# Optimization experiments

Hardware: AMD Instinct MI355X
Metric: run time of the kernel (lower is better)

The kernel has to match this reference:

```python
import jax, jax.numpy as jnp
import numpy as np

BETA = 1e10  # hard softmax temperature from the original module


def setup_inputs() -> dict:
    key = jax.random.key(0)
    ks = jax.random.split(key, 7)
    bs, nc, units, feat = 128, 1024, 512, 512
    return {
        "x": jax.random.normal(ks[0], (bs, feat), jnp.float32),
        "class_logits": jax.random.normal(ks[1], (bs, nc), jnp.float32),
        "h_states": jax.random.normal(ks[2], (nc, units), jnp.float32) * 0.1,
        "c_states": jax.random.normal(ks[3], (nc, units), jnp.float32) * 0.1,
        "kernel": jax.random.normal(ks[4], (feat, 4 * units), jnp.float32) * 0.05,
        "rec_kernel": jax.random.normal(ks[5], (units, 4 * units), jnp.float32) * 0.05,
        "bias": jnp.zeros((4 * units,), jnp.float32),
    }


def _diff_scatter(A, B, w):
    # A: (nc, u) old class states, B: (bs, u) new states, w: (bs, nc) hard softmax.
    # Faithful to tf version: broadcast to (nc, bs, u), blend, then reduce_max over bs.
    m = w.T[:, :, None]                       # (nc, bs, 1)
    blended = A[:, None, :] * (1.0 - m) + B[None, :, :] * m  # (nc, bs, u)
    return jnp.max(blended, axis=1)           # (nc, u)


def reference(x, class_logits, h_states, c_states, kernel, rec_kernel, bias):
    # diff_gather: softmax-weighted sum over classes == weights @ params
    w = jax.nn.softmax(class_logits * BETA, axis=-1)  # (bs, nc), ~one-hot
    h0 = w @ h_states                                  # (bs, u)
    c0 = w @ c_states                                  # (bs, u)

    # single-step Keras LSTM (seq_len == 1): gate order i, f, c, o
    z = x @ kernel + h0 @ rec_kernel + bias            # (bs, 4u)
    i, f, g, o = jnp.split(z, 4, axis=-1)
    i = jax.nn.sigmoid(i)
    f = jax.nn.sigmoid(f)
    g = jnp.tanh(g)
    o = jax.nn.sigmoid(o)
    c = f * c0 + i * g
    h = o * jnp.tanh(c)                                # LSTM output == h

    new_h = _diff_scatter(h_states, h, w)
    new_c = _diff_scatter(c_states, c, w)
    return h, new_h, new_c
```

## Files before the change

kernel.cpp:

```cpp
#include <hip/hip_runtime.h>
#include <hip/hip_bf16.h>
#include <math.h>

#define BS    128
#define NC    1024
#define UNITS 512
#define FEAT  512
#define FOURU 2048
#define KG    4
#define NT    32
#define WPAD  40

typedef short  bf16x8 __attribute__((ext_vector_type(8)));
typedef float  f32x4  __attribute__((ext_vector_type(4)));

__device__ __forceinline__ unsigned short bf_rhu(float f) {
    union { float f; unsigned u; } v; v.f = f;
    return (unsigned short)((v.u + 0x8000u) >> 16);
}
__device__ __forceinline__ unsigned pack2(float a, float b) {
    return (unsigned)bf_rhu(a) | ((unsigned)bf_rhu(b) << 16);
}

__global__ __launch_bounds__(256) void argmax_prep_kernel(
    const float* __restrict__ logits, const float* __restrict__ x,
    const float* __restrict__ h_states,
    int* __restrict__ sidx, unsigned* __restrict__ Abf )
{
    int b = blockIdx.x;
    int t = threadIdx.x;
    float best = -INFINITY; int bi = 0;
    for (int i = t; i < NC; i += 256) {
        float v = logits[b * NC + i];
        if (v > best) { best = v; bi = i; }
    }
    for (int off = 32; off > 0; off >>= 1) {
        float ov = __shfl_down(best, off);
        int   oi = __shfl_down(bi, off);
        if (ov > best || (ov == best && oi < bi)) { best = ov; bi = oi; }
    }
    __shared__ float sv[4]; __shared__ int si[4];
    __shared__ int sbi;
    int wid = t >> 6;
    if ((t & 63) == 0) { sv[wid] = best; si[wid] = bi; }
    __syncthreads();
    if (t == 0) {
        for (int w = 1; w < 4; ++w)
            if (sv[w] > best || (sv[w] == best && si[w] < bi)) { best = sv[w]; bi = si[w]; }
        sidx[b] = bi;
        sbi = bi;
    }
    __syncthreads();
    int st = t & 127;
    const float* srcrow = (t < 128) ? (x + (long)b * FEAT)
                                    : (h_states + (long)sbi * UNITS);
    float4 v = *(const float4*)(srcrow + st * 4);
    unsigned lo = pack2(v.x, v.y), hi = pack2(v.z, v.w);
    unsigned du = (unsigned)b * 512u + (t < 128 ? 0u : 256u) + (unsigned)st * 2u;
    *(uint2*)(Abf + du) = make_uint2(lo, hi);
}

__global__ __launch_bounds__(256) void gemm_kernel(
    const unsigned short* __restrict__ Abf,
    const float* __restrict__ kern, const float* __restrict__ reck,
    float* __restrict__ z_part)
{
    __shared__ __align__(16) unsigned short as[BS * 32];
    __shared__ __align__(16) unsigned short wst[NT * WPAD];

    int t = threadIdx.x;
    int ntile = blockIdx.x * NT;
    int kg = blockIdx.y;
    const float* W = (kg < 2) ? kern : reck;
    int wk0base = (kg & 1) * 256;
    int k0base  = kg * 256;

    int wid = t >> 6, lane = t & 63;
    int l15 = lane & 15, quad = lane >> 4;

    f32x4 zero = {0.f, 0.f, 0.f, 0.f};
    f32x4 acc[2][2] = {{zero, zero}, {zero, zero}};

    #pragma unroll
    for (int kstep = 0; kstep < 8; ++kstep) {
        int k0  = k0base  + kstep * 32;
        int wk0 = wk0base + kstep * 32;

        for (int r = 0; r < 2; ++r) {
            int G = r * 256 + t;
            int m = G >> 2;
            int p = G & 3;
            int c = (p ^ (m >> 1)) & 3;
            bf16x8 v = *(const bf16x8*)(Abf + (long)m * 1024 + k0 + c * 8);
            *(bf16x8*)&as[G * 8] = v;
        }
        for (int p = 0; p < 4; ++p) {
            int kk = (t >> 5) + p * 8;
            int n  = t & 31;
            wst[n * WPAD + kk] = bf_rhu(W[(long)(wk0 + kk) * FOURU + ntile + n]);
        }
        __syncthreads();

        bf16x8 afrag[2], bfrag[2];
        for (int ms = 0; ms < 2; ++ms) {
            int m = wid * 32 + ms * 16 + l15;
            afrag[ms] = *(const bf16x8*)&as[(m * 4 + ((quad ^ (m >> 1)) & 3)) * 8];
        }
        for (int ns = 0; ns < 2; ++ns) {
            int n = ns * 16 + l15;
            bfrag[ns] = *(const bf16x8*)&wst[n * WPAD + quad * 8];
        }
        for (int ms = 0; ms < 2; ++ms)
            for (int ns = 0; ns < 2; ++ns)
                acc[ms][ns] = __builtin_amdgcn_mfma_f32_16x16x32_bf16(
                                  afrag[ms], bfrag[ns], acc[ms][ns], 0, 0, 0);
        __syncthreads();
    }

    float* zp = z_part + (long)kg * BS * FOURU;
    #pragma unroll
    for (int ms = 0; ms < 2; ++ms)
        #pragma unroll
        for (int ns = 0; ns < 2; ++ns)
            #pragma unroll
            for (int r = 0; r < 4; ++r) {
                int m = wid * 32 + ms * 16 + quad * 4 + r;
                int n = ntile + ns * 16 + l15;
                zp[(long)m * FOURU + n] = acc[ms][ns][r];
            }
}

__global__ __launch_bounds__(256) void scatter_lstm_kernel(
    const float* __restrict__ z_part, const float* __restrict__ bias,
    const float* __restrict__ h_states, const float* __restrict__ c_states,
    const int* __restrict__ sidx,
    float* __restrict__ h_out, float* __restrict__ out_h, float* __restrict__ out_c)
{
    __shared__ int s[BS];
    int t = threadIdx.x;
    if (t < BS) s[t] = sidx[t];
    __syncthreads();
    int j = blockIdx.x >> 1;
    int u = (blockIdx.x & 1) * 256 + t;

    float ah = h_states[(long)j * UNITS + u];
    float ac = c_states[(long)j * UNITS + u];

    float mh = -INFINITY, mc = -INFINITY;
    int count = 0;
    float bi_ = bias[u], bf_ = bias[512 + u], bg_ = bias[1024 + u], bo_ = bias[1536 + u];

    for (int b = 0; b < BS; ++b) {
        if (s[b] == j) {
            ++count;
            float zi = bi_, zf = bf_, zg = bg_, zo = bo_;
            #pragma unroll
            for (int kg = 0; kg < KG; ++kg) {
                const float* zp = z_part + (long)kg * BS * FOURU + (long)b * FOURU;
                zi += zp[u];
                zf += zp[512 + u];
                zg += zp[1024 + u];
                zo += zp[1536 + u];
            }
            float ig = 1.f / (1.f + expf(-zi));
            float fg = 1.f / (1.f + expf(-zf));
            float gg = tanhf(zg);
            float og = 1.f / (1.f + expf(-zo));
            float c  = fg * ac + ig * gg;
            float h  = og * tanhf(c);
            h_out[(long)b * UNITS + u] = h;
            mh = fmaxf(mh, h);
            mc = fmaxf(mc, c);
        }
    }
    out_h[(long)j * UNITS + u] = (count == BS) ? mh : fmaxf(ah, mh);
    out_c[(long)j * UNITS + u] = (count == BS) ? mc : fmaxf(ac, mc);
}

extern "C" void kernel_launch(void* const* d_in, const int* in_sizes, int n_in,
                              void* d_out, int out_size, void* d_ws, size_t ws_size,
                              hipStream_t stream)
{
    (void)in_sizes; (void)n_in; (void)out_size; (void)ws_size;
    const float* x      = (const float*)d_in[0];
    const float* logits = (const float*)d_in[1];
    const float* h_st   = (const float*)d_in[2];
    const float* c_st   = (const float*)d_in[3];
    const float* kern   = (const float*)d_in[4];
    const float* reck   = (const float*)d_in[5];
    const float* bias   = (const float*)d_in[6];

    float* out        = (float*)d_out;
    float* out_h_step = out;
    float* out_newh   = out + BS * UNITS;
    float* out_newc   = out + BS * UNITS + NC * UNITS;

    char*     ws     = (char*)d_ws;
    int*      sidx   = (int*)ws;
    unsigned* Abf    = (unsigned*)(ws + 1024);
    float*    z_part = (float*)(ws + 1024 * 1024);

    argmax_prep_kernel<<<BS, 256, 0, stream>>>(logits, x, h_st, sidx, Abf);
    gemm_kernel<<<dim3(FOURU / NT, KG), 256, 0, stream>>>(
        (const unsigned short*)Abf, kern, reck, z_part);
    scatter_lstm_kernel<<<NC * UNITS / 256, 256, 0, stream>>>(
        z_part, bias, h_st, c_st, sidx, out_h_step, out_newh, out_newc);
}
```

Baseline: 111.1 us.

## Pre-transpose weights to bf16 in prep kernel and drop LDS staging in GEMM

The prep kernel gains extra blocks that convert both weight matrices to bf16 in a transposed (n-major, k-contiguous) layout in the workspace. The GEMM then loads A and W fragments straight from global memory with no shared-memory staging or barriers. The K split grows from 4 to 8 groups, so the scatter kernel sums 8 partial results, giving more GEMM blocks. In exchange the weights are written to and read back from the workspace each call, adding an extra pass over them, and the scatter has more partials to read.

```diff
diff --git a/kernel.cpp b/kernel.cpp
--- a/kernel.cpp
+++ b/kernel.cpp
@@ -7,12 +7,10 @@
 #define UNITS 512
 #define FEAT  512
 #define FOURU 2048
-#define KG    4
-#define NT    32
-#define WPAD  40
-
-typedef short  bf16x8 __attribute__((ext_vector_type(8)));
-typedef float  f32x4  __attribute__((ext_vector_type(4)));
+#define KG    8
+
+typedef short bf16x8 __attribute__((ext_vector_type(8)));
+typedef float f32x4  __attribute__((ext_vector_type(4)));
 
 __device__ __forceinline__ unsigned short bf_rhu(float f) {
     union { float f; unsigned u; } v; v.f = f;
@@ -22,99 +20,96 @@
     return (unsigned)bf_rhu(a) | ((unsigned)bf_rhu(b) << 16);
 }
 
-__global__ __launch_bounds__(256) void argmax_prep_kernel(
+__global__ __launch_bounds__(256) void prep_kernel(
     const float* __restrict__ logits, const float* __restrict__ x,
-    const float* __restrict__ h_states,
-    int* __restrict__ sidx, unsigned* __restrict__ Abf )
-{
-    int b = blockIdx.x;
-    int t = threadIdx.x;
-    float best = -INFINITY; int bi = 0;
-    for (int i = t; i < NC; i += 256) {
-        float v = logits[b * NC + i];
-        if (v > best) { best = v; bi = i; }
+    const float* __restrict__ h_st,
+    const float* __restrict__ kern, const float* __restrict__ reck,
+    int* __restrict__ sidx,
+    unsigned short* __restrict__ Abf,
+    unsigned short* __restrict__ Wt)
+{
+    const int bid = blockIdx.x, t = threadIdx.x;
+    const int wid = t >> 6, lane = t & 63;
+
+    if (bid < BS) {
+        int b = bid;
+        float best = -INFINITY; int bi = 0;
+        for (int i = t; i < NC; i += 256) {
+            float v = logits[b * NC + i];
+            if (v > best) { best = v; bi = i; }
+        }
+        for (int off = 32; off > 0; off >>= 1) {
+            float ov = __shfl_down(best, off);
+            int   oi = __shfl_down(bi, off);
+            if (ov > best || (ov == best && oi < bi)) { best = ov; bi = oi; }
+        }
+        __shared__ float sv[4]; __shared__ int si[4]; __shared__ int sbi;
+        if ((t & 63) == 0) { sv[wid] = best; si[wid] = bi; }
+        __syncthreads();
+        if (t == 0) {
+            for (int w = 1; w < 4; ++w)
+                if (sv[w] > best || (sv[w] == best && si[w] < bi)) { best = sv[w]; bi = si[w]; }
+            sidx[b] = bi;
+            sbi = bi;
+        }
+        __syncthreads();
+        int st = t & 127;
+        const float* srcrow = (t < 128) ? (x + (long)b * FEAT)
+                                        : (h_st + (long)sbi * UNITS);
+        float4 v = *(const float4*)(srcrow + st * 4);
+        unsigned lo = pack2(v.x, v.y), hi = pack2(v.z, v.w);
+        unsigned du = (unsigned)b * 512u + (t < 128 ? 0u : 256u) + (unsigned)st * 2u;
+        *(uint2*)((unsigned*)Abf + du) = make_uint2(lo, hi);
+    } else {
+        int gw = (bid - BS) * 4 + wid;
+        for (int task = gw; task < 4096; task += 1536) {
+            int kc = task >> 5;
+            int n  = (task & 31) * 64 + lane;
+            int r0 = kc * 8;
+            const float* base = (r0 < 512) ? (kern + (long)r0 * FOURU + n)
+                                           : (reck + (long)(r0 - 512) * FOURU + n);
+            bf16x8 o;
+            #pragma unroll
+            for (int j = 0; j < 8; ++j)
+                o[j] = (short)bf_rhu(base[(long)j * FOURU]);
+            *(bf16x8*)(Wt + (long)n * 1024 + r0) = o;
+        }
     }
-    for (int off = 32; off > 0; off >>= 1) {
-        float ov = __shfl_down(best, off);
-        int   oi = __shfl_down(bi, off);
-        if (ov > best || (ov == best && oi < bi)) { best = ov; bi = oi; }
-    }
-    __shared__ float sv[4]; __shared__ int si[4];
-    __shared__ int sbi;
-    int wid = t >> 6;
-    if ((t & 63) == 0) { sv[wid] = best; si[wid] = bi; }
-    __syncthreads();
-    if (t == 0) {
-        for (int w = 1; w < 4; ++w)
-            if (sv[w] > best || (sv[w] == best && si[w] < bi)) { best = sv[w]; bi = si[w]; }
-        sidx[b] = bi;
-        sbi = bi;
-    }
-    __syncthreads();
-    int st = t & 127;
-    const float* srcrow = (t < 128) ? (x + (long)b * FEAT)
-                                    : (h_states + (long)sbi * UNITS);
-    float4 v = *(const float4*)(srcrow + st * 4);
-    unsigned lo = pack2(v.x, v.y), hi = pack2(v.z, v.w);
-    unsigned du = (unsigned)b * 512u + (t < 128 ? 0u : 256u) + (unsigned)st * 2u;
-    *(uint2*)(Abf + du) = make_uint2(lo, hi);
 }
 
 __global__ __launch_bounds__(256) void gemm_kernel(
     const unsigned short* __restrict__ Abf,
-    const float* __restrict__ kern, const float* __restrict__ reck,
+    const unsigned short* __restrict__ Wt,
     float* __restrict__ z_part)
 {
-    __shared__ __align__(16) unsigned short as[BS * 32];
-    __shared__ __align__(16) unsigned short wst[NT * WPAD];
-
-    int t = threadIdx.x;
-    int ntile = blockIdx.x * NT;
-    int kg = blockIdx.y;
-    const float* W = (kg < 2) ? kern : reck;
-    int wk0base = (kg & 1) * 256;
-    int k0base  = kg * 256;
-
-    int wid = t >> 6, lane = t & 63;
-    int l15 = lane & 15, quad = lane >> 4;
+    const int t = threadIdx.x;
+    const int wid = t >> 6, lane = t & 63, l15 = lane & 15, quad = lane >> 4;
+    const int nt = blockIdx.x & 63, kg = blockIdx.x >> 6;
+    const int k0base = kg * 128 + quad * 8;
 
     f32x4 zero = {0.f, 0.f, 0.f, 0.f};
     f32x4 acc[2][2] = {{zero, zero}, {zero, zero}};
 
     #pragma unroll
-    for (int kstep = 0; kstep < 8; ++kstep) {
-        int k0  = k0base  + kstep * 32;
-        int wk0 = wk0base + kstep * 32;
-
-        for (int r = 0; r < 2; ++r) {
-            int G = r * 256 + t;
-            int m = G >> 2;
-            int p = G & 3;
-            int c = (p ^ (m >> 1)) & 3;
-            bf16x8 v = *(const bf16x8*)(Abf + (long)m * 1024 + k0 + c * 8);
-            *(bf16x8*)&as[G * 8] = v;
-        }
-        for (int p = 0; p < 4; ++p) {
-            int kk = (t >> 5) + p * 8;
-            int n  = t & 31;
-            wst[n * WPAD + kk] = bf_rhu(W[(long)(wk0 + kk) * FOURU + ntile + n]);
-        }
-        __syncthreads();
-
-        bf16x8 afrag[2], bfrag[2];
+    for (int kstep = 0; kstep < 4; ++kstep) {
+        int k0 = k0base + kstep * 32;
+        bf16x8 af[2], wf[2];
+        #pragma unroll
         for (int ms = 0; ms < 2; ++ms) {
             int m = wid * 32 + ms * 16 + l15;
-            afrag[ms] = *(const bf16x8*)&as[(m * 4 + ((quad ^ (m >> 1)) & 3)) * 8];
-        }
+            af[ms] = *(const bf16x8*)(Abf + (long)m * 1024 + k0);
+        }
+        #pragma unroll
         for (int ns = 0; ns < 2; ++ns) {
-            int n = ns * 16 + l15;
-            bfrag[ns] = *(const bf16x8*)&wst[n * WPAD + quad * 8];
-        }
+            int n = nt * 32 + ns * 16 + l15;
+            wf[ns] = *(const bf16x8*)(Wt + (long)n * 1024 + k0);
+        }
+        #pragma unroll
         for (int ms = 0; ms < 2; ++ms)
+            #pragma unroll
             for (int ns = 0; ns < 2; ++ns)
                 acc[ms][ns] = __builtin_amdgcn_mfma_f32_16x16x32_bf16(
-                                  afrag[ms], bfrag[ns], acc[ms][ns], 0, 0, 0);
-        __syncthreads();
+                                  af[ms], wf[ns], acc[ms][ns], 0, 0, 0);
     }
 
     float* zp = z_part + (long)kg * BS * FOURU;
@@ -125,7 +120,7 @@
             #pragma unroll
             for (int r = 0; r < 4; ++r) {
                 int m = wid * 32 + ms * 16 + quad * 4 + r;
-                int n = ntile + ns * 16 + l15;
+                int n = nt * 32 + ns * 16 + l15;
                 zp[(long)m * FOURU + n] = acc[ms][ns][r];
             }
 }
@@ -195,14 +190,14 @@
     float* out_newh   = out + BS * UNITS;
     float* out_newc   = out + BS * UNITS + NC * UNITS;
 
-    char*     ws     = (char*)d_ws;
-    int*      sidx   = (int*)ws;
-    unsigned* Abf    = (unsigned*)(ws + 1024);
-    float*    z_part = (float*)(ws + 1024 * 1024);
-
-    argmax_prep_kernel<<<BS, 256, 0, stream>>>(logits, x, h_st, sidx, Abf);
-    gemm_kernel<<<dim3(FOURU / NT, KG), 256, 0, stream>>>(
-        (const unsigned short*)Abf, kern, reck, z_part);
+    char*           ws     = (char*)d_ws;
+    int*            sidx   = (int*)ws;
+    unsigned short* Abf    = (unsigned short*)(ws + 4096);
+    float*          z_part = (float*)(ws + (1u << 20));
+    unsigned short* Wt     = (unsigned short*)(ws + 10u * (1u << 20));
+
+    prep_kernel<<<512, 256, 0, stream>>>(logits, x, h_st, kern, reck, sidx, Abf, Wt);
+    gemm_kernel<<<512, 256, 0, stream>>>(Abf, Wt, z_part);
     scatter_lstm_kernel<<<NC * UNITS / 256, 256, 0, stream>>>(
         z_part, bias, h_st, c_st, sidx, out_h_step, out_newh, out_newc);
 }
```

New measurement: 103.3 us. 7.1% less time.
